# Performance work log

Measured on AMD Instinct MI355X. Metric: run time of the kernel, lower is better.

Reference implementation:

```python
import jax, jax.numpy as jnp
import numpy as np

B, T, H = 1024, 128, 256
EPS = 1e-5


def _lstm(x, W_ih, W_hh, b_ih, b_hh):
    # x: [B,T,D] -> hs: [B,T,H], hn: [B,H]; PyTorch gate order i,f,g,o
    xp = jnp.einsum('btd,gd->btg', x, W_ih) + b_ih + b_hh  # [B,T,4H]
    h0 = jnp.zeros((x.shape[0], W_hh.shape[1]), x.dtype)

    def step(carry, xt):
        h, c = carry
        g = xt + h @ W_hh.T
        i, f, gg, o = jnp.split(g, 4, axis=-1)
        c = jax.nn.sigmoid(f) * c + jax.nn.sigmoid(i) * jnp.tanh(gg)
        h = jax.nn.sigmoid(o) * jnp.tanh(c)
        return (h, c), h

    (hn, _), hs = jax.lax.scan(step, (h0, h0), jnp.swapaxes(xp, 0, 1))
    return jnp.swapaxes(hs, 0, 1), hn


def _bn(x, g, b, m, v):
    # eval-mode BatchNorm1d
    return g * (x - m) * jax.lax.rsqrt(v + EPS) + b


def setup_inputs() -> dict:
    key = jax.random.key(0)
    ks = jax.random.split(key, 40)
    f = lambda i, shape, s=0.05: jax.random.normal(ks[i], shape, jnp.float32) * s
    d = {}
    d['seq_cont_data'] = f(0, (B, T, 64), 1.0)
    d['seq_cat_data'] = jax.random.randint(ks[1], (B, T, 2), 0, 500)
    d['non_seq_cat_data'] = jax.random.randint(ks[2], (B, 2), 0, 1000)
    d['non_seq_cont_data'] = f(3, (B, 32), 1.0)
    d['emb_ns0'] = f(4, (10000, 64))
    d['emb_ns1'] = f(5, (1000, 64))
    d['emb_s0'] = f(6, (1000, 32))
    d['emb_s1'] = f(7, (500, 32))
    d['W_ih'] = f(8, (4 * H, 128)); d['W_hh'] = f(9, (4 * H, H))
    d['b_ih'] = f(10, (4 * H,)); d['b_hh'] = f(11, (4 * H,))
    d['W_ltd'] = f(12, (H, H)); d['b_ltd'] = f(13, (H,))
    d['W_conv'] = f(14, (H, T)); d['b_conv'] = f(15, (H,))
    d['W_tpa'] = f(16, (H, H)); d['W_tpa_h'] = f(17, (H, H)); d['W_tpa_c'] = f(18, (H, H))
    FIN = 672
    d['W_f1'] = f(19, (512, FIN)); d['b_f1'] = f(20, (512,))
    d['g1'] = 1.0 + f(21, (512,)); d['be1'] = f(22, (512,)); d['m1'] = f(23, (512,)); d['v1'] = jnp.ones((512,), jnp.float32)
    d['W_f2'] = f(24, (256, 512)); d['b_f2'] = f(25, (256,))
    d['g2'] = 1.0 + f(26, (256,)); d['be2'] = f(27, (256,)); d['m2'] = f(28, (256,)); d['v2'] = jnp.ones((256,), jnp.float32)
    d['W_out'] = f(29, (64, 256)); d['b_out'] = f(30, (64,))
    return d


def reference(seq_cont_data, seq_cat_data, non_seq_cat_data, non_seq_cont_data,
              emb_ns0, emb_ns1, emb_s0, emb_s1,
              W_ih, W_hh, b_ih, b_hh, W_ltd, b_ltd, W_conv, b_conv,
              W_tpa, W_tpa_h, W_tpa_c,
              W_f1, b_f1, g1, be1, m1, v1,
              W_f2, b_f2, g2, be2, m2, v2,
              W_out, b_out):
    # non-sequential input: embeddings + continuous
    ns_cat = jnp.concatenate([emb_ns0[non_seq_cat_data[:, 0]], emb_ns1[non_seq_cat_data[:, 1]]], axis=1)
    non_seq_inp = jnp.concatenate([ns_cat, non_seq_cont_data], axis=1)  # [B,160]
    # sequential input: embeddings + continuous
    s_cat = jnp.concatenate([emb_s0[seq_cat_data[:, :, 0]], emb_s1[seq_cat_data[:, :, 1]]], axis=2)
    seq_data = jnp.concatenate([s_cat, seq_cont_data], axis=2)  # [B,T,128]
    output, hn = _lstm(seq_data, W_ih, W_hh, b_ih, b_hh)  # [B,T,H], [B,H]
    # TPA: hc[b,i,j] = Conv1d_j(output[:,:,i]) = sum_t output[b,t,i]*W_conv[j,t] + b_conv[j]
    hc = jnp.einsum('bti,jt->bij', output, W_conv) + b_conv  # [B,H,H]
    # alpha[b,i] = sigmoid( (hc[b,i] @ W_tpa.T) . hn[b] )
    alpha = jax.nn.sigmoid(jnp.einsum('bik,bk->bi', jnp.einsum('bij,kj->bik', hc, W_tpa), hn))
    vt = jnp.einsum('bi,bih->bh', alpha, hc)  # [B,H]
    htprime = hn @ W_tpa_h.T + vt @ W_tpa_c.T
    seq_inp = hn @ W_ltd.T + b_ltd
    fin_input = jnp.concatenate([non_seq_inp, seq_inp, htprime], axis=1)  # [B,672]
    x = _bn(jax.nn.relu(fin_input @ W_f1.T + b_f1), g1, be1, m1, v1)
    x = _bn(jax.nn.relu(x @ W_f2.T + b_f2), g2, be2, m2, v2)
    x = jax.nn.relu(x @ W_out.T + b_out)
    return x, fin_input
```

## Files before the change

kernel.cpp:

```cpp
#include <hip/hip_runtime.h>
#include <hip/hip_bf16.h>
#include <math.h>

#define B_SZ 1024
#define T_SZ 128
#define H_SZ 256
#define DIN  128
#define G4   1024
#define FINW 672

using bf16   = __hip_bfloat16;
using short4v = __attribute__((ext_vector_type(4))) short;
using short8 = __attribute__((ext_vector_type(8))) short;
using f32x4  = __attribute__((ext_vector_type(4))) float;

__device__ __forceinline__ float bf2f(bf16 x) { return __bfloat162float(x); }
__device__ __forceinline__ bf16  f2bf(float x) { return __float2bfloat16(x); }
__device__ __forceinline__ float sigm(float x) { return 1.0f / (1.0f + __expf(-x)); }
__device__ __forceinline__ float ftanh(float x) { return 2.0f / (1.0f + __expf(-2.0f * x)) - 1.0f; }
__device__ __forceinline__ float bfraw2f(unsigned short r) {
  unsigned u = ((unsigned)r) << 16;
  return *reinterpret_cast<float*>(&u);
}

struct Ptrs { const void* p[33]; };

#define NSEG 30
__device__ __host__ constexpr int kSegOffArr(int i) {
  constexpr int off[NSEG + 1] = {
      0,       32768,   672768,  736768,  768768,  784768,  915840,
      1177984, 1179008, 1180032, 1245568, 1245824, 1278592, 1278848,
      1344384, 1409920, 1475456, 1819520, 1820032, 1820544, 1821056,
      1821568, 1822080, 1953152, 1953408, 1953664, 1953920, 1954176,
      1954432, 1970816, 1970880};
  return off[i];
}
#define ARENA_TOTAL 1970880

__global__ __launch_bounds__(256) void k_convert(Ptrs pk, bf16* __restrict__ dst) {
  bool isf32 = ((((const unsigned*)pk.p[24])[0] & 0xFFFFu) == 0u);
  int stride = gridDim.x * blockDim.x;
  for (int i = blockIdx.x * blockDim.x + threadIdx.x; i < ARENA_TOTAL; i += stride) {
    int s = 0, base = 0;
#pragma unroll
    for (int j = 1; j < NSEG; j++) {
      bool ge = (i >= kSegOffArr(j));
      s    = ge ? j : s;
      base = ge ? kSegOffArr(j) : base;
    }
    int off = i - base;
    const void* src = pk.p[3 + s];
    dst[i] = isf32 ? f2bf(((const float*)src)[off]) : ((const bf16*)src)[off];
  }
}

__global__ __launch_bounds__(256) void k_gather(
    const void* __restrict__ seq_cont_raw, const int* __restrict__ seq_cat,
    const bf16* __restrict__ emb_s0, const bf16* __restrict__ emb_s1,
    bf16* __restrict__ seq_out, const unsigned* __restrict__ probe) {
  bool isf32 = ((probe[0] & 0xFFFFu) == 0u);
  int gid = blockIdx.x * blockDim.x + threadIdx.x;
  int seg = gid & 15;
  int m   = gid >> 4;
  int t   = m >> 10;
  int b   = m & 1023;
  bf16* dst = seq_out + (long)m * DIN + seg * 8;
  if (seg < 8) {
    const bf16* src;
    if (seg < 4) {
      int idx = seq_cat[(b * T_SZ + t) * 2 + 0];
      src = emb_s0 + idx * 32 + seg * 8;
    } else {
      int idx = seq_cat[(b * T_SZ + t) * 2 + 1];
      src = emb_s1 + idx * 32 + (seg - 4) * 8;
    }
    *reinterpret_cast<short8*>(dst) = *reinterpret_cast<const short8*>(src);
  } else {
    long base = ((long)b * T_SZ + t) * 64 + (seg - 8) * 8;
    if (isf32) {
      const float4* sp =
          reinterpret_cast<const float4*>((const float*)seq_cont_raw + base);
      float4 x0 = sp[0], x1 = sp[1];
      union { short8 v; bf16 h[8]; } u;
      u.h[0] = f2bf(x0.x); u.h[1] = f2bf(x0.y); u.h[2] = f2bf(x0.z); u.h[3] = f2bf(x0.w);
      u.h[4] = f2bf(x1.x); u.h[5] = f2bf(x1.y); u.h[6] = f2bf(x1.z); u.h[7] = f2bf(x1.w);
      *reinterpret_cast<short8*>(dst) = u.v;
    } else {
      *reinterpret_cast<short8*>(dst) =
          *reinterpret_cast<const short8*>((const bf16*)seq_cont_raw + base);
    }
  }
}

#define HPOISON 0xFFFFFFFFu
__global__ __launch_bounds__(512, 2) void k_lstm(
    const bf16* __restrict__ seq, const bf16* __restrict__ Wih,
    const bf16* __restrict__ Whh, const bf16* __restrict__ bih,
    const bf16* __restrict__ bhh, bf16* __restrict__ hs) {
  __shared__ short8 hsh[2][8 * 64];
  __shared__ short8 xsh[2][4 * 64];
  int tid  = threadIdx.x;
  int w    = tid >> 6, lane = tid & 63;
  int quad = lane >> 4, l15 = lane & 15;
  int bid  = blockIdx.x;
  int gid  = bid & 63;
  int rank = bid >> 6;
  int peer = 1 - rank;
  long b0  = (long)gid * 16;
  int hup = w * 16 + l15;
  int hu  = rank * 128 + hup;

  { short8 z = {0,0,0,0,0,0,0,0}; hsh[0][tid] = z; }

  float bia[4];
#pragma unroll
  for (int i = 0; i < 4; ++i) {
    int grow = i * H_SZ + hu;
    bia[i] = bf2f(bih[grow]) + bf2f(bhh[grow]);
  }

  short8 wif[4][4];
  short8 whfS[4][4];
  short8 whfP[4][4];
#pragma unroll
  for (int i = 0; i < 4; ++i) {
    long grow = (long)(i * H_SZ + rank * 128 + hup);
#pragma unroll
    for (int kt = 0; kt < 4; ++kt) {
      wif[i][kt] = *reinterpret_cast<const short8*>(
          Wih + grow * DIN + kt * 32 + quad * 8);
      whfS[i][kt] = *reinterpret_cast<const short8*>(
          Whh + grow * H_SZ + (rank * 4 + kt) * 32 + quad * 8);
      whfP[i][kt] = *reinterpret_cast<const short8*>(
          Whh + grow * H_SZ + (peer * 4 + kt) * 32 + quad * 8);
    }
  }
  if (tid < 256)
    xsh[0][tid] = *reinterpret_cast<const short8*>(
        seq + (b0 + (tid & 15)) * DIN + (tid >> 6) * 32 +
        ((tid >> 4) & 3) * 8);
  float c[4] = {0.f, 0.f, 0.f, 0.f};
  __syncthreads();

#define LGKM_BARRIER() do { \
    asm volatile("s_waitcnt lgkmcnt(0)" ::: "memory"); \
    __builtin_amdgcn_s_barrier(); } while (0)

  for (int t = 0; t < T_SZ; ++t) {
    int cur = t & 1, nxt = cur ^ 1;
    short8 xpre;
    bool dopre = (t + 1 < T_SZ) & (tid < 256);
    if (dopre)
      xpre = *reinterpret_cast<const short8*>(
          seq + ((long)(t + 1) * B_SZ + b0 + (tid & 15)) * DIN +
          (tid >> 6) * 32 + ((tid >> 4) & 3) * 8);

    f32x4 acc[4];
#pragma unroll
    for (int i = 0; i < 4; ++i) acc[i] = {0.f, 0.f, 0.f, 0.f};

#pragma unroll
    for (int kt = 0; kt < 4; ++kt) {
      short8 ax = xsh[cur][kt * 64 + lane];
#pragma unroll
      for (int i = 0; i < 4; ++i)
        acc[i] = __builtin_amdgcn_mfma_f32_16x16x32_bf16(ax, wif[i][kt], acc[i], 0, 0, 0);
    }
#pragma unroll
    for (int kt = 0; kt < 4; ++kt) {
      short8 ah = hsh[cur][(rank * 4 + kt) * 64 + lane];
#pragma unroll
      for (int i = 0; i < 4; ++i)
        acc[i] = __builtin_amdgcn_mfma_f32_16x16x32_bf16(ah, whfS[i][kt], acc[i], 0, 0, 0);
    }

    if (t > 0) {
      if (tid < 256) {
        int m = tid >> 4, seg = tid & 15;
        const unsigned* src = reinterpret_cast<const unsigned*>(
            hs + ((long)(t - 1) * B_SZ + b0 + m) * H_SZ + peer * 128 + seg * 8);
        unsigned d0, d1, d2, d3;
        do {
          d0 = __hip_atomic_load(src + 0, __ATOMIC_RELAXED, __HIP_MEMORY_SCOPE_AGENT);
          d1 = __hip_atomic_load(src + 1, __ATOMIC_RELAXED, __HIP_MEMORY_SCOPE_AGENT);
          d2 = __hip_atomic_load(src + 2, __ATOMIC_RELAXED, __HIP_MEMORY_SCOPE_AGENT);
          d3 = __hip_atomic_load(src + 3, __ATOMIC_RELAXED, __HIP_MEMORY_SCOPE_AGENT);
        } while (d0 == HPOISON || d1 == HPOISON || d2 == HPOISON || d3 == HPOISON);
        union { unsigned u[4]; short8 s; } cv;
        cv.u[0] = d0; cv.u[1] = d1; cv.u[2] = d2; cv.u[3] = d3;
        hsh[cur][(peer * 4 + (seg >> 2)) * 64 + (seg & 3) * 16 + m] = cv.s;
      }
      LGKM_BARRIER();
    }
#pragma unroll
    for (int kt = 0; kt < 4; ++kt) {
      short8 ah = hsh[cur][(peer * 4 + kt) * 64 + lane];
#pragma unroll
      for (int i = 0; i < 4; ++i)
        acc[i] = __builtin_amdgcn_mfma_f32_16x16x32_bf16(ah, whfP[i][kt], acc[i], 0, 0, 0);
    }

    bf16* hbn = reinterpret_cast<bf16*>(&hsh[nxt][0]);
#pragma unroll
    for (int r = 0; r < 4; ++r) {
      float iv = sigm(acc[0][r] + bia[0]);
      float fv = sigm(acc[1][r] + bia[1]);
      float gv = ftanh(acc[2][r] + bia[2]);
      float ov = sigm(acc[3][r] + bia[3]);
      c[r] = fv * c[r] + iv * gv;
      bf16 hv = f2bf(ov * ftanh(c[r]));
      int m = quad * 4 + r;
      hbn[(((hu >> 5) * 64) + ((hu >> 3) & 3) * 16 + m) * 8 + (hu & 7)] = hv;
      unsigned hraw = (unsigned)*reinterpret_cast<unsigned short*>(&hv);
      unsigned nb = (unsigned)__shfl_down((int)hraw, 1, 64);
      if ((l15 & 1) == 0) {
        unsigned* dst = reinterpret_cast<unsigned*>(
            hs + ((long)t * B_SZ + b0 + m) * H_SZ + hu);
        __hip_atomic_store(dst, hraw | (nb << 16), __ATOMIC_RELAXED,
                           __HIP_MEMORY_SCOPE_AGENT);
      }
    }
    if (dopre) xsh[nxt][tid] = xpre;
    LGKM_BARRIER();
  }
#undef LGKM_BARRIER
}

__global__ __launch_bounds__(256) void k_u(
    const bf16* __restrict__ hs, const bf16* __restrict__ W_tpa,
    const bf16* __restrict__ W_conv, const bf16* __restrict__ b_conv,
    float* __restrict__ w2, float* __restrict__ c0) {
  __shared__ float hn_sh[8][256];
  __shared__ float u_sh[8][256];
  __shared__ float wred[4][8];
  int tid = threadIdx.x;
  long b0 = (long)blockIdx.x * 8;
#pragma unroll
  for (int r = 0; r < 8; r++)
    hn_sh[r][tid] = bf2f(hs[((long)(T_SZ - 1) * B_SZ + b0 + r) * H_SZ + tid]);
  __syncthreads();
  float u[8] = {0,0,0,0,0,0,0,0};
  for (int k = 0; k < H_SZ; k++) {
    float wv = bf2f(W_tpa[k * H_SZ + tid]);
#pragma unroll
    for (int r = 0; r < 8; r++) u[r] += hn_sh[r][k] * wv;
  }
  float bc = bf2f(b_conv[tid]);
  float p[8];
#pragma unroll
  for (int r = 0; r < 8; r++) { u_sh[r][tid] = u[r]; p[r] = u[r] * bc; }
#pragma unroll
  for (int d = 32; d > 0; d >>= 1)
#pragma unroll
    for (int r = 0; r < 8; r++) p[r] += __shfl_down(p[r], d, 64);
  if ((tid & 63) == 0)
#pragma unroll
    for (int r = 0; r < 8; r++) wred[tid >> 6][r] = p[r];
  __syncthreads();
  if (tid < 8)
    c0[b0 + tid] = wred[0][tid] + wred[1][tid] + wred[2][tid] + wred[3][tid];
  if (tid < T_SZ) {
    float a[8] = {0,0,0,0,0,0,0,0};
    for (int j = 0; j < H_SZ; j++) {
      float wv = bf2f(W_conv[j * T_SZ + tid]);
#pragma unroll
      for (int r = 0; r < 8; r++) a[r] += u_sh[r][j] * wv;
    }
#pragma unroll
    for (int r = 0; r < 8; r++) w2[(b0 + r) * T_SZ + tid] = a[r];
  }
}

__global__ __launch_bounds__(256) void k_alphas(
    const bf16* __restrict__ hs, const float* __restrict__ w2,
    const float* __restrict__ c0, float* __restrict__ asum,
    float* __restrict__ sbuf) {
  __shared__ unsigned hc[128 * 129];
  __shared__ float w2s[T_SZ];
  __shared__ float ash[H_SZ];
  __shared__ float red[256];
  int b = blockIdx.x, tid = threadIdx.x;
#pragma unroll
  for (int p = 0; p < 16; p++) {
    int task = p * 256 + tid;
    int row = task >> 5, seg = task & 31;
    short8 v = *reinterpret_cast<const short8*>(
        hs + ((long)row * B_SZ + b) * H_SZ + seg * 8);
    union { short8 s; unsigned u[4]; } cv; cv.s = v;
#pragma unroll
    for (int k = 0; k < 4; k++) hc[row * 129 + seg * 4 + k] = cv.u[k];
  }
  if (tid < T_SZ) w2s[tid] = w2[b * T_SZ + tid];
  __syncthreads();
  {
    float ap = c0[b];
    int wi = tid >> 1, hi = tid & 1;
    for (int t = 0; t < T_SZ; t++) {
      unsigned uv = hc[t * 129 + wi];
      unsigned short h16 = hi ? (unsigned short)(uv >> 16) : (unsigned short)(uv & 0xFFFF);
      float hvf = __bfloat162float(*reinterpret_cast<bf16*>(&h16));
      ap += hvf * w2s[t];
    }
    float a = sigm(ap);
    ash[tid] = a;
    red[tid] = a;
  }
  __syncthreads();
  for (int s = 128; s > 0; s >>= 1) {
    if (tid < s) red[tid] += red[tid + s];
    __syncthreads();
  }
  if (tid == 0) asum[b] = red[0];
  if (tid < T_SZ) {
    float acc = 0.f;
    for (int k = 0; k < 128; k++) {
      int wi = (k + tid) & 127;
      unsigned uv = hc[tid * 129 + wi];
      unsigned short lo16 = (unsigned short)(uv & 0xFFFF);
      unsigned short hi16 = (unsigned short)(uv >> 16);
      float lo = __bfloat162float(*reinterpret_cast<bf16*>(&lo16));
      float hi = __bfloat162float(*reinterpret_cast<bf16*>(&hi16));
      acc += ash[2 * wi] * lo + ash[2 * wi + 1] * hi;
    }
    sbuf[b * T_SZ + tid] = acc;
  }
}

__global__ __launch_bounds__(256) void k_fin(
    const bf16* __restrict__ hs, const float* __restrict__ sbuf,
    const float* __restrict__ asum, const bf16* __restrict__ W_conv,
    const bf16* __restrict__ b_conv, const bf16* __restrict__ W_tpa_h,
    const bf16* __restrict__ W_tpa_c, const bf16* __restrict__ W_ltd,
    const bf16* __restrict__ b_ltd, const int* __restrict__ ns_cat,
    const bf16* __restrict__ emb_ns0, const bf16* __restrict__ emb_ns1,
    const bf16* __restrict__ ns_cont, float* __restrict__ fin,
    void* __restrict__ d_out_raw, const unsigned* __restrict__ probe) {
  bool isf32 = ((probe[0] & 0xFFFFu) == 0u);
  __shared__ float s_sh[8][128];
  __shared__ float hn_sh[8][256];
  __shared__ float vt_sh[8][256];
  int tid = threadIdx.x;
  long b0 = (long)blockIdx.x * 8;
  auto store2 = [&](int r, int pos, float v) {
    fin[(b0 + r) * FINW + pos] = v;
    if (isf32)
      ((float*)d_out_raw + 65536)[(b0 + r) * FINW + pos] = v;
    else
      ((bf16*)d_out_raw + 65536)[(b0 + r) * FINW + pos] = f2bf(v);
  };
  if (tid < 128)
#pragma unroll
    for (int r = 0; r < 8; r++) s_sh[r][tid] = sbuf[(b0 + r) * T_SZ + tid];
#pragma unroll
  for (int r = 0; r < 8; r++)
    hn_sh[r][tid] = bf2f(hs[((long)(T_SZ - 1) * B_SZ + b0 + r) * H_SZ + tid]);
  __syncthreads();
  float vt[8] = {0,0,0,0,0,0,0,0};
  for (int t = 0; t < T_SZ; t++) {
    float wv = bf2f(W_conv[tid * T_SZ + t]);
#pragma unroll
    for (int r = 0; r < 8; r++) vt[r] += wv * s_sh[r][t];
  }
  float bc = bf2f(b_conv[tid]);
#pragma unroll
  for (int r = 0; r < 8; r++) {
    vt[r] += bc * asum[b0 + r];
    vt_sh[r][tid] = vt[r];
  }
  __syncthreads();
  float htp[8] = {0,0,0,0,0,0,0,0}, sq[8] = {0,0,0,0,0,0,0,0};
  for (int k = 0; k < H_SZ; k++) {
    float whk = bf2f(W_tpa_h[tid * H_SZ + k]);
    float wck = bf2f(W_tpa_c[tid * H_SZ + k]);
    float wlk = bf2f(W_ltd[tid * H_SZ + k]);
#pragma unroll
    for (int r = 0; r < 8; r++) {
      htp[r] += hn_sh[r][k] * whk + vt_sh[r][k] * wck;
      sq[r]  += hn_sh[r][k] * wlk;
    }
  }
  float bl = bf2f(b_ltd[tid]);
#pragma unroll
  for (int r = 0; r < 8; r++) {
    store2(r, 160 + tid, sq[r] + bl);
    store2(r, 416 + tid, htp[r]);
  }
  if (tid < 160) {
#pragma unroll
    for (int r = 0; r < 8; r++) {
      long b = b0 + r;
      float v;
      if (tid < 64)       v = bf2f(emb_ns0[(long)ns_cat[b * 2 + 0] * 64 + tid]);
      else if (tid < 128) v = bf2f(emb_ns1[(long)ns_cat[b * 2 + 1] * 64 + tid - 64]);
      else                v = bf2f(ns_cont[b * 32 + tid - 128]);
      store2(r, tid, v);
    }
  }
}

__global__ __launch_bounds__(512) void k_mlp(
    const float* __restrict__ fin, const bf16* __restrict__ W_f1,
    const bf16* __restrict__ b_f1, const bf16* __restrict__ g1,
    const bf16* __restrict__ be1, const bf16* __restrict__ m1,
    const bf16* __restrict__ v1, const bf16* __restrict__ W_f2,
    const bf16* __restrict__ b_f2, const bf16* __restrict__ g2,
    const bf16* __restrict__ be2, const bf16* __restrict__ m2,
    const bf16* __restrict__ v2, const bf16* __restrict__ W_out,
    const bf16* __restrict__ b_out, void* __restrict__ d_out_raw,
    const unsigned* __restrict__ probe) {
  bool isf32 = ((probe[0] & 0xFFFFu) == 0u);
  __shared__ float a_sh[FINW * 8];
  __shared__ float x1t[512 * 8];
  __shared__ float x2t[256 * 8];
  int tid = threadIdx.x;
  long b0 = (long)blockIdx.x * 8;
  for (int i = tid; i < 8 * FINW; i += 512) {
    int r = i / FINW, k = i - r * FINW;
    a_sh[k * 8 + r] = fin[b0 * FINW + i];
  }
  __syncthreads();
  {
    int n = tid;
    float acc[8] = {0, 0, 0, 0, 0, 0, 0, 0};
    const short4v* wr4 = reinterpret_cast<const short4v*>(W_f1 + (long)n * FINW);
    for (int kk = 0; kk < FINW / 4; kk++) {
      short4v w4 = wr4[kk];
#pragma unroll
      for (int j = 0; j < 4; j++) {
        float wv = bfraw2f((unsigned short)w4[j]);
        const float4* ap = reinterpret_cast<const float4*>(&a_sh[(kk * 4 + j) * 8]);
        float4 a0 = ap[0], a1 = ap[1];
        acc[0] += wv * a0.x; acc[1] += wv * a0.y;
        acc[2] += wv * a0.z; acc[3] += wv * a0.w;
        acc[4] += wv * a1.x; acc[5] += wv * a1.y;
        acc[6] += wv * a1.z; acc[7] += wv * a1.w;
      }
    }
    float bb = bf2f(b_f1[n]);
    float scale = bf2f(g1[n]) * rsqrtf(bf2f(v1[n]) + 1e-5f);
    float mm = bf2f(m1[n]), bee = bf2f(be1[n]);
#pragma unroll
    for (int r = 0; r < 8; r++) {
      float x = acc[r] + bb;
      x = x > 0.f ? x : 0.f;
      x1t[n * 8 + r] = (x - mm) * scale + bee;
    }
  }
  __syncthreads();
  if (tid < 256) {
    int n = tid;
    float acc[8] = {0, 0, 0, 0, 0, 0, 0, 0};
    const short8* wr8 = reinterpret_cast<const short8*>(W_f2 + (long)n * 512);
    for (int kk = 0; kk < 64; kk++) {
      short8 w8 = wr8[kk];
#pragma unroll
      for (int j = 0; j < 8; j++) {
        float wv = bfraw2f((unsigned short)w8[j]);
        const float4* ap = reinterpret_cast<const float4*>(&x1t[(kk * 8 + j) * 8]);
        float4 a0 = ap[0], a1 = ap[1];
        acc[0] += wv * a0.x; acc[1] += wv * a0.y;
        acc[2] += wv * a0.z; acc[3] += wv * a0.w;
        acc[4] += wv * a1.x; acc[5] += wv * a1.y;
        acc[6] += wv * a1.z; acc[7] += wv * a1.w;
      }
    }
    float bb = bf2f(b_f2[n]);
    float scale = bf2f(g2[n]) * rsqrtf(bf2f(v2[n]) + 1e-5f);
    float mm = bf2f(m2[n]), bee = bf2f(be2[n]);
#pragma unroll
    for (int r = 0; r < 8; r++) {
      float x = acc[r] + bb;
      x = x > 0.f ? x : 0.f;
      x2t[n * 8 + r] = (x - mm) * scale + bee;
    }
  }
  __syncthreads();
  if (tid < 64) {
    int n = tid;
    float acc[8] = {0, 0, 0, 0, 0, 0, 0, 0};
    const short8* wr8 = reinterpret_cast<const short8*>(W_out + (long)n * H_SZ);
    for (int kk = 0; kk < 32; kk++) {
      short8 w8 = wr8[kk];
#pragma unroll
      for (int j = 0; j < 8; j++) {
        float wv = bfraw2f((unsigned short)w8[j]);
        const float4* ap = reinterpret_cast<const float4*>(&x2t[(kk * 8 + j) * 8]);
        float4 a0 = ap[0], a1 = ap[1];
        acc[0] += wv * a0.x; acc[1] += wv * a0.y;
        acc[2] += wv * a0.z; acc[3] += wv * a0.w;
        acc[4] += wv * a1.x; acc[5] += wv * a1.y;
        acc[6] += wv * a1.z; acc[7] += wv * a1.w;
      }
    }
    float bb = bf2f(b_out[n]);
#pragma unroll
    for (int r = 0; r < 8; r++) {
      float x = acc[r] + bb;
      x = x > 0.f ? x : 0.f;
      if (isf32)
        ((float*)d_out_raw)[(b0 + r) * 64 + n] = x;
      else
        ((bf16*)d_out_raw)[(b0 + r) * 64 + n] = f2bf(x);
    }
  }
}

extern "C" void kernel_launch(void* const* d_in, const int* in_sizes, int n_in,
                              void* d_out, int out_size, void* d_ws,
                              size_t ws_size, hipStream_t stream) {
  const int* seq_cat = (const int*)d_in[1];
  const int* ns_cat  = (const int*)d_in[2];
  const unsigned* probe = (const unsigned*)d_in[24];

  char* ws = (char*)d_ws;
  bf16* seqd  = (bf16*)ws;  ws += (size_t)T_SZ * B_SZ * DIN * 2;
  bf16* hsb   = (bf16*)ws;  ws += (size_t)T_SZ * B_SZ * H_SZ * 2;
  bf16* arena = (bf16*)ws;  ws += (size_t)ARENA_TOTAL * 2;
  float* w2   = (float*)ws; ws += (size_t)B_SZ * T_SZ * 4;
  float* c0   = (float*)ws; ws += (size_t)B_SZ * 4;
  float* asum = (float*)ws; ws += (size_t)B_SZ * 4;
  float* sbuf = (float*)ws; ws += (size_t)B_SZ * T_SZ * 4;
  float* fin  = (float*)ws; ws += (size_t)B_SZ * FINW * 4;

  const bf16* c_ns_cont = arena + 0;
  const bf16* c_emb_ns0 = arena + 32768;
  const bf16* c_emb_ns1 = arena + 672768;
  const bf16* c_emb_s0  = arena + 736768;
  const bf16* c_emb_s1  = arena + 768768;
  const bf16* c_W_ih    = arena + 784768;
  const bf16* c_W_hh    = arena + 915840;
  const bf16* c_b_ih    = arena + 1177984;
  const bf16* c_b_hh    = arena + 1179008;
  const bf16* c_W_ltd   = arena + 1180032;
  const bf16* c_b_ltd   = arena + 1245568;
  const bf16* c_W_conv  = arena + 1245824;
  const bf16* c_b_conv  = arena + 1278592;
  const bf16* c_W_tpa   = arena + 1278848;
  const bf16* c_W_tpa_h = arena + 1344384;
  const bf16* c_W_tpa_c = arena + 1409920;
  const bf16* c_W_f1    = arena + 1475456;
  const bf16* c_b_f1    = arena + 1819520;
  const bf16* c_g1      = arena + 1820032;
  const bf16* c_be1     = arena + 1820544;
  const bf16* c_m1      = arena + 1821056;
  const bf16* c_v1      = arena + 1821568;
  const bf16* c_W_f2    = arena + 1822080;
  const bf16* c_b_f2    = arena + 1953152;
  const bf16* c_g2      = arena + 1953408;
  const bf16* c_be2     = arena + 1953664;
  const bf16* c_m2      = arena + 1953920;
  const bf16* c_v2      = arena + 1954176;
  const bf16* c_W_out   = arena + 1954432;
  const bf16* c_b_out   = arena + 1970816;

  Ptrs pk;
  for (int i = 0; i < 33; i++) pk.p[i] = d_in[i];

  hipMemsetAsync(hsb, 0xFF, (size_t)T_SZ * B_SZ * H_SZ * 2, stream);
  k_convert<<<dim3(512), 256, 0, stream>>>(pk, arena);
  k_gather<<<dim3(B_SZ * T_SZ * 16 / 256), 256, 0, stream>>>(
      d_in[0], seq_cat, c_emb_s0, c_emb_s1, seqd, probe);
  k_lstm<<<dim3(128), 512, 0, stream>>>(seqd, c_W_ih, c_W_hh, c_b_ih, c_b_hh,
                                        hsb);
  k_u<<<dim3(B_SZ / 8), 256, 0, stream>>>(hsb, c_W_tpa, c_W_conv, c_b_conv, w2, c0);
  k_alphas<<<dim3(B_SZ), 256, 0, stream>>>(hsb, w2, c0, asum, sbuf);
  k_fin<<<dim3(B_SZ / 8), 256, 0, stream>>>(hsb, sbuf, asum, c_W_conv, c_b_conv,
                                            c_W_tpa_h, c_W_tpa_c, c_W_ltd,
                                            c_b_ltd, ns_cat, c_emb_ns0,
                                            c_emb_ns1, c_ns_cont, fin, d_out,
                                            probe);
  k_mlp<<<dim3(B_SZ / 8), 512, 0, stream>>>(fin, c_W_f1, c_b_f1, c_g1, c_be1,
                                            c_m1, c_v1, c_W_f2, c_b_f2, c_g2,
                                            c_be2, c_m2, c_v2, c_W_out, c_b_out,
                                            d_out, probe);
}
```

Baseline: 716.5 us.

## Pre-transpose TPA/LTD/conv weights, fuse poison fill into convert, batch LSTM stores

The convert kernel now also writes transposed copies of W_tpa_h, W_tpa_c, W_ltd and W_conv, so k_fin can read weights coalesced across threads instead of with a row stride. The separate memset of the hidden-state buffer is folded into the convert kernel. The matvec loops in k_u and k_fin are blocked by 8 and use float4 shared-memory reads. In the LSTM step, the global h stores move after the barrier and the custom lgkm barrier is replaced with __syncthreads. This adds conversion work and arena space, and the reordered stores may change how soon peer blocks see h.

New measurement: 682.7 us. 4.7% less time.

```diff
diff --git a/kernel.cpp b/kernel.cpp
--- a/kernel.cpp
+++ b/kernel.cpp
@@ -10,7 +10,6 @@
 #define FINW 672
 
 using bf16   = __hip_bfloat16;
-using short4v = __attribute__((ext_vector_type(4))) short;
 using short8 = __attribute__((ext_vector_type(8))) short;
 using f32x4  = __attribute__((ext_vector_type(4))) float;
 
@@ -36,11 +35,20 @@
   return off[i];
 }
 #define ARENA_TOTAL 1970880
-
-__global__ __launch_bounds__(256) void k_convert(Ptrs pk, bf16* __restrict__ dst) {
+#define TR_BASE   1970880
+#define TR_WthT   0
+#define TR_WtcT   65536
+#define TR_WltT   131072
+#define TR_WcvT   196608
+#define TR_TOTAL  229376
+#define ARENA_TOTAL2 (ARENA_TOTAL + TR_TOTAL)
+
+__global__ __launch_bounds__(256) void k_convert(Ptrs pk, bf16* __restrict__ dst,
+                                                 uint4* __restrict__ hsp) {
   bool isf32 = ((((const unsigned*)pk.p[24])[0] & 0xFFFFu) == 0u);
   int stride = gridDim.x * blockDim.x;
-  for (int i = blockIdx.x * blockDim.x + threadIdx.x; i < ARENA_TOTAL; i += stride) {
+  int gtid = blockIdx.x * blockDim.x + threadIdx.x;
+  for (int i = gtid; i < ARENA_TOTAL; i += stride) {
     int s = 0, base = 0;
 #pragma unroll
     for (int j = 1; j < NSEG; j++) {
@@ -52,6 +60,18 @@
     const void* src = pk.p[3 + s];
     dst[i] = isf32 ? f2bf(((const float*)src)[off]) : ((const bf16*)src)[off];
   }
+  for (int j = gtid; j < TR_TOTAL; j += stride) {
+    const void* src;
+    int off;
+    if (j < TR_WtcT)      { src = pk.p[17]; int jj = j;            off = (jj & 255) * 256 + (jj >> 8); }
+    else if (j < TR_WltT) { src = pk.p[18]; int jj = j - TR_WtcT;  off = (jj & 255) * 256 + (jj >> 8); }
+    else if (j < TR_WcvT) { src = pk.p[12]; int jj = j - TR_WltT;  off = (jj & 255) * 256 + (jj >> 8); }
+    else                  { src = pk.p[14]; int jj = j - TR_WcvT;  off = (jj & 255) * 128 + (jj >> 8); }
+    dst[TR_BASE + j] = isf32 ? f2bf(((const float*)src)[off]) : ((const bf16*)src)[off];
+  }
+  uint4 pv = make_uint4(0xFFFFFFFFu, 0xFFFFFFFFu, 0xFFFFFFFFu, 0xFFFFFFFFu);
+  for (int i = gtid; i < (int)((size_t)T_SZ * B_SZ * H_SZ * 2 / 16); i += stride)
+    hsp[i] = pv;
 }
 
 __global__ __launch_bounds__(256) void k_gather(
@@ -142,10 +162,6 @@
   float c[4] = {0.f, 0.f, 0.f, 0.f};
   __syncthreads();
 
-#define LGKM_BARRIER() do { \
-    asm volatile("s_waitcnt lgkmcnt(0)" ::: "memory"); \
-    __builtin_amdgcn_s_barrier(); } while (0)
-
   for (int t = 0; t < T_SZ; ++t) {
     int cur = t & 1, nxt = cur ^ 1;
     short8 xpre;
@@ -190,7 +206,7 @@
         cv.u[0] = d0; cv.u[1] = d1; cv.u[2] = d2; cv.u[3] = d3;
         hsh[cur][(peer * 4 + (seg >> 2)) * 64 + (seg & 3) * 16 + m] = cv.s;
       }
-      LGKM_BARRIER();
+      __syncthreads();
     }
 #pragma unroll
     for (int kt = 0; kt < 4; ++kt) {
@@ -201,6 +217,7 @@
     }
 
     bf16* hbn = reinterpret_cast<bf16*>(&hsh[nxt][0]);
+    unsigned hpk[4];
 #pragma unroll
     for (int r = 0; r < 4; ++r) {
       float iv = sigm(acc[0][r] + bia[0]);
@@ -213,17 +230,21 @@
       hbn[(((hu >> 5) * 64) + ((hu >> 3) & 3) * 16 + m) * 8 + (hu & 7)] = hv;
       unsigned hraw = (unsigned)*reinterpret_cast<unsigned short*>(&hv);
       unsigned nb = (unsigned)__shfl_down((int)hraw, 1, 64);
-      if ((l15 & 1) == 0) {
+      hpk[r] = hraw | (nb << 16);
+    }
+    if (dopre) xsh[nxt][tid] = xpre;
+    __syncthreads();
+    if ((l15 & 1) == 0) {
+#pragma unroll
+      for (int r = 0; r < 4; ++r) {
+        int m = quad * 4 + r;
         unsigned* dst = reinterpret_cast<unsigned*>(
             hs + ((long)t * B_SZ + b0 + m) * H_SZ + hu);
-        __hip_atomic_store(dst, hraw | (nb << 16), __ATOMIC_RELAXED,
+        __hip_atomic_store(dst, hpk[r], __ATOMIC_RELAXED,
                            __HIP_MEMORY_SCOPE_AGENT);
       }
     }
-    if (dopre) xsh[nxt][tid] = xpre;
-    LGKM_BARRIER();
-  }
-#undef LGKM_BARRIER
+  }
 }
 
 __global__ __launch_bounds__(256) void k_u(
@@ -240,10 +261,20 @@
     hn_sh[r][tid] = bf2f(hs[((long)(T_SZ - 1) * B_SZ + b0 + r) * H_SZ + tid]);
   __syncthreads();
   float u[8] = {0,0,0,0,0,0,0,0};
-  for (int k = 0; k < H_SZ; k++) {
-    float wv = bf2f(W_tpa[k * H_SZ + tid]);
-#pragma unroll
-    for (int r = 0; r < 8; r++) u[r] += hn_sh[r][k] * wv;
+  for (int kk = 0; kk < 32; kk++) {
+    float wv[8];
+#pragma unroll
+    for (int q = 0; q < 8; q++)
+      wv[q] = bf2f(W_tpa[(kk * 8 + q) * H_SZ + tid]);
+#pragma unroll
+    for (int r = 0; r < 8; r++) {
+      const float4* hp = reinterpret_cast<const float4*>(&hn_sh[r][kk * 8]);
+      float4 h0 = hp[0], h1 = hp[1];
+      u[r] += h0.x * wv[0]; u[r] += h0.y * wv[1];
+      u[r] += h0.z * wv[2]; u[r] += h0.w * wv[3];
+      u[r] += h1.x * wv[4]; u[r] += h1.y * wv[5];
+      u[r] += h1.z * wv[6]; u[r] += h1.w * wv[7];
+    }
   }
   float bc = bf2f(b_conv[tid]);
   float p[8];
@@ -261,10 +292,20 @@
     c0[b0 + tid] = wred[0][tid] + wred[1][tid] + wred[2][tid] + wred[3][tid];
   if (tid < T_SZ) {
     float a[8] = {0,0,0,0,0,0,0,0};
-    for (int j = 0; j < H_SZ; j++) {
-      float wv = bf2f(W_conv[j * T_SZ + tid]);
-#pragma unroll
-      for (int r = 0; r < 8; r++) a[r] += u_sh[r][j] * wv;
+    for (int jj = 0; jj < 32; jj++) {
+      float wv[8];
+#pragma unroll
+      for (int q = 0; q < 8; q++)
+        wv[q] = bf2f(W_conv[(jj * 8 + q) * T_SZ + tid]);
+#pragma unroll
+      for (int r = 0; r < 8; r++) {
+        const float4* up = reinterpret_cast<const float4*>(&u_sh[r][jj * 8]);
+        float4 u0 = up[0], u1 = up[1];
+        a[r] += u0.x * wv[0]; a[r] += u0.y * wv[1];
+        a[r] += u0.z * wv[2]; a[r] += u0.w * wv[3];
+        a[r] += u1.x * wv[4]; a[r] += u1.y * wv[5];
+        a[r] += u1.z * wv[6]; a[r] += u1.w * wv[7];
+      }
     }
 #pragma unroll
     for (int r = 0; r < 8; r++) w2[(b0 + r) * T_SZ + tid] = a[r];
@@ -328,9 +369,9 @@
 
 __global__ __launch_bounds__(256) void k_fin(
     const bf16* __restrict__ hs, const float* __restrict__ sbuf,
-    const float* __restrict__ asum, const bf16* __restrict__ W_conv,
-    const bf16* __restrict__ b_conv, const bf16* __restrict__ W_tpa_h,
-    const bf16* __restrict__ W_tpa_c, const bf16* __restrict__ W_ltd,
+    const float* __restrict__ asum, const bf16* __restrict__ WcvT,
+    const bf16* __restrict__ b_conv, const bf16* __restrict__ WthT,
+    const bf16* __restrict__ WtcT, const bf16* __restrict__ WltT,
     const bf16* __restrict__ b_ltd, const int* __restrict__ ns_cat,
     const bf16* __restrict__ emb_ns0, const bf16* __restrict__ emb_ns1,
     const bf16* __restrict__ ns_cont, float* __restrict__ fin,
@@ -356,10 +397,20 @@
     hn_sh[r][tid] = bf2f(hs[((long)(T_SZ - 1) * B_SZ + b0 + r) * H_SZ + tid]);
   __syncthreads();
   float vt[8] = {0,0,0,0,0,0,0,0};
-  for (int t = 0; t < T_SZ; t++) {
-    float wv = bf2f(W_conv[tid * T_SZ + t]);
-#pragma unroll
-    for (int r = 0; r < 8; r++) vt[r] += wv * s_sh[r][t];
+  for (int tt = 0; tt < 16; tt++) {
+    float wv[8];
+#pragma unroll
+    for (int q = 0; q < 8; q++)
+      wv[q] = bf2f(WcvT[(tt * 8 + q) * H_SZ + tid]);
+#pragma unroll
+    for (int r = 0; r < 8; r++) {
+      const float4* sp = reinterpret_cast<const float4*>(&s_sh[r][tt * 8]);
+      float4 s0 = sp[0], s1 = sp[1];
+      vt[r] += wv[0] * s0.x; vt[r] += wv[1] * s0.y;
+      vt[r] += wv[2] * s0.z; vt[r] += wv[3] * s0.w;
+      vt[r] += wv[4] * s1.x; vt[r] += wv[5] * s1.y;
+      vt[r] += wv[6] * s1.z; vt[r] += wv[7] * s1.w;
+    }
   }
   float bc = bf2f(b_conv[tid]);
 #pragma unroll
@@ -369,14 +420,28 @@
   }
   __syncthreads();
   float htp[8] = {0,0,0,0,0,0,0,0}, sq[8] = {0,0,0,0,0,0,0,0};
-  for (int k = 0; k < H_SZ; k++) {
-    float whk = bf2f(W_tpa_h[tid * H_SZ + k]);
-    float wck = bf2f(W_tpa_c[tid * H_SZ + k]);
-    float wlk = bf2f(W_ltd[tid * H_SZ + k]);
+  for (int kk = 0; kk < 32; kk++) {
+    float wh[8], wc[8], wl[8];
+#pragma unroll
+    for (int q = 0; q < 8; q++) {
+      int k = kk * 8 + q;
+      wh[q] = bf2f(WthT[k * H_SZ + tid]);
+      wc[q] = bf2f(WtcT[k * H_SZ + tid]);
+      wl[q] = bf2f(WltT[k * H_SZ + tid]);
+    }
 #pragma unroll
     for (int r = 0; r < 8; r++) {
-      htp[r] += hn_sh[r][k] * whk + vt_sh[r][k] * wck;
-      sq[r]  += hn_sh[r][k] * wlk;
+      const float4* hp = reinterpret_cast<const float4*>(&hn_sh[r][kk * 8]);
+      const float4* vp = reinterpret_cast<const float4*>(&vt_sh[r][kk * 8]);
+      float4 h0 = hp[0], h1 = hp[1], v0 = vp[0], v1 = vp[1];
+      htp[r] += h0.x * wh[0] + v0.x * wc[0]; sq[r] += h0.x * wl[0];
+      htp[r] += h0.y * wh[1] + v0.y * wc[1]; sq[r] += h0.y * wl[1];
+      htp[r] += h0.z * wh[2] + v0.z * wc[2]; sq[r] += h0.z * wl[2];
+      htp[r] += h0.w * wh[3] + v0.w * wc[3]; sq[r] += h0.w * wl[3];
+      htp[r] += h1.x * wh[4] + v1.x * wc[4]; sq[r] += h1.x * wl[4];
+      htp[r] += h1.y * wh[5] + v1.y * wc[5]; sq[r] += h1.y * wl[5];
+      htp[r] += h1.z * wh[6] + v1.z * wc[6]; sq[r] += h1.z * wl[6];
+      htp[r] += h1.w * wh[7] + v1.w * wc[7]; sq[r] += h1.w * wl[7];
     }
   }
   float bl = bf2f(b_ltd[tid]);
@@ -398,6 +463,7 @@
   }
 }
 
+using short4v = __attribute__((ext_vector_type(4))) short;
 __global__ __launch_bounds__(512) void k_mlp(
     const float* __restrict__ fin, const bf16* __restrict__ W_f1,
     const bf16* __restrict__ b_f1, const bf16* __restrict__ g1,
@@ -515,7 +581,7 @@
   char* ws = (char*)d_ws;
   bf16* seqd  = (bf16*)ws;  ws += (size_t)T_SZ * B_SZ * DIN * 2;
   bf16* hsb   = (bf16*)ws;  ws += (size_t)T_SZ * B_SZ * H_SZ * 2;
-  bf16* arena = (bf16*)ws;  ws += (size_t)ARENA_TOTAL * 2;
+  bf16* arena = (bf16*)ws;  ws += (size_t)ARENA_TOTAL2 * 2;
   float* w2   = (float*)ws; ws += (size_t)B_SZ * T_SZ * 4;
   float* c0   = (float*)ws; ws += (size_t)B_SZ * 4;
   float* asum = (float*)ws; ws += (size_t)B_SZ * 4;
@@ -531,13 +597,10 @@
   const bf16* c_W_hh    = arena + 915840;
   const bf16* c_b_ih    = arena + 1177984;
   const bf16* c_b_hh    = arena + 1179008;
-  const bf16* c_W_ltd   = arena + 1180032;
   const bf16* c_b_ltd   = arena + 1245568;
-  const bf16* c_W_conv  = arena + 1245824;
   const bf16* c_b_conv  = arena + 1278592;
   const bf16* c_W_tpa   = arena + 1278848;
-  const bf16* c_W_tpa_h = arena + 1344384;
-  const bf16* c_W_tpa_c = arena + 1409920;
+  const bf16* c_W_conv  = arena + 1245824;
   const bf16* c_W_f1    = arena + 1475456;
   const bf16* c_b_f1    = arena + 1819520;
   const bf16* c_g1      = arena + 1820032;
@@ -552,20 +615,23 @@
   const bf16* c_v2      = arena + 1954176;
   const bf16* c_W_out   = arena + 1954432;
   const bf16* c_b_out   = arena + 1970816;
+  const bf16* c_WthT    = arena + TR_BASE + TR_WthT;
+  const bf16* c_WtcT    = arena + TR_BASE + TR_WtcT;
+  const bf16* c_WltT    = arena + TR_BASE + TR_WltT;
+  const bf16* c_WcvT    = arena + TR_BASE + TR_WcvT;
 
   Ptrs pk;
   for (int i = 0; i < 33; i++) pk.p[i] = d_in[i];
 
-  hipMemsetAsync(hsb, 0xFF, (size_t)T_SZ * B_SZ * H_SZ * 2, stream);
-  k_convert<<<dim3(512), 256, 0, stream>>>(pk, arena);
+  k_convert<<<dim3(512), 256, 0, stream>>>(pk, arena, (uint4*)hsb);
   k_gather<<<dim3(B_SZ * T_SZ * 16 / 256), 256, 0, stream>>>(
       d_in[0], seq_cat, c_emb_s0, c_emb_s1, seqd, probe);
   k_lstm<<<dim3(128), 512, 0, stream>>>(seqd, c_W_ih, c_W_hh, c_b_ih, c_b_hh,
                                         hsb);
   k_u<<<dim3(B_SZ / 8), 256, 0, stream>>>(hsb, c_W_tpa, c_W_conv, c_b_conv, w2, c0);
   k_alphas<<<dim3(B_SZ), 256, 0, stream>>>(hsb, w2, c0, asum, sbuf);
-  k_fin<<<dim3(B_SZ / 8), 256, 0, stream>>>(hsb, sbuf, asum, c_W_conv, c_b_conv,
-                                            c_W_tpa_h, c_W_tpa_c, c_W_ltd,
+  k_fin<<<dim3(B_SZ / 8), 256, 0, stream>>>(hsb, sbuf, asum, c_WcvT, c_b_conv,
+                                            c_WthT, c_WtcT, c_WltT,
                                             c_b_ltd, ns_cat, c_emb_ns0,
                                             c_emb_ns1, c_ns_cont, fin, d_out,
                                             probe);
```
